# Optimization experiments

Hardware: AMD Instinct MI355X
Metric: run time of the kernel (lower is better)

Reference implementation:

```python
import jax, jax.numpy as jnp
import numpy as np

N = 100000
E = 1600000
IN_DIM = 128
HID_DIM = 128
NUM_CLASSES = 40


def setup_inputs() -> dict:
    key = jax.random.key(0)
    k1, k2, k3, k4, k5, k6 = jax.random.split(key, 6)
    x = jax.random.normal(k1, (N, IN_DIM), dtype=jnp.float32)
    e = jax.random.randint(k2, (2, E), 0, N, dtype=jnp.int64)
    s1 = 1.0 / np.sqrt(IN_DIM)
    s2 = 1.0 / np.sqrt(HID_DIM)
    W1 = jax.random.uniform(k3, (IN_DIM, HID_DIM), jnp.float32, -s1, s1)
    b1 = jax.random.uniform(k4, (HID_DIM,), jnp.float32, -s1, s1)
    W2 = jax.random.uniform(k5, (HID_DIM, NUM_CLASSES), jnp.float32, -s2, s2)
    b2 = jax.random.uniform(k6, (NUM_CLASSES,), jnp.float32, -s2, s2)
    return {"x": x, "e": e, "W1": W1, "b1": b1, "W2": W2, "b2": b2}


def _gcn_conv(x, src, dst, norm, W, b, n):
    # linear transform first (PyG GCNConv), then normalized aggregation
    h = x @ W                                    # [N, d_out]
    out = jax.ops.segment_sum(h[src] * norm[:, None], dst, num_segments=n)
    return out + b


def reference(x, e, W1, b1, W2, b2):
    n = x.shape[0]
    loop = jnp.arange(n, dtype=e.dtype)
    src = jnp.concatenate([e[0], loop])          # add self-loops
    dst = jnp.concatenate([e[1], loop])
    deg = jax.ops.segment_sum(jnp.ones_like(dst, dtype=x.dtype), dst, num_segments=n)
    d_inv_sqrt = deg ** -0.5                     # deg >= 1 due to self-loops
    norm = d_inv_sqrt[src] * d_inv_sqrt[dst]     # symmetric normalization
    h = jax.nn.relu(_gcn_conv(x, src, dst, norm, W1, b1, n))
    return _gcn_conv(h, src, dst, norm, W2, b2, n)
```

## Files before the change

kernel.cpp:

```cpp
#include <hip/hip_runtime.h>


typedef unsigned int u32;
typedef unsigned short u16;
typedef __attribute__((ext_vector_type(8))) short short8;
typedef __attribute__((ext_vector_type(4))) float floatx4;

#define CHUNK 8192

static __device__ inline u16 f2bf(float f) {
    u32 u = __float_as_uint(f);
    return (u16)((u + 0x7FFFu + ((u >> 16) & 1u)) >> 16);
}
static __device__ inline u32 pack2(float a, float b) {
    return (u32)f2bf(a) | ((u32)f2bf(b) << 16);
}
static __device__ inline float bflo(u32 u) { return __uint_as_float(u << 16); }
static __device__ inline float bfhi(u32 u) { return __uint_as_float(u & 0xffff0000u); }

__global__ void k_detect(const int* __restrict__ e32, int* __restrict__ flag) {
    int t = threadIdx.x;
    if (e32[2 * t + 1] != 0) atomicOr(flag, 1);
}

__global__ void k_prepW(const float* __restrict__ W1, const float* __restrict__ W2,
                        u16* __restrict__ WTb, u16* __restrict__ W2Tb) {
    int id = blockIdx.x * 256 + threadIdx.x;
    if (id < 16384) {
        int k = id >> 7, c = id & 127;
        WTb[c * 128 + k] = f2bf(W1[id]);
    } else {
        int id2 = id - 16384;
        if (id2 < 6144) {
            int c = id2 >> 7, k = id2 & 127;
            W2Tb[id2] = f2bf(c < 40 ? W2[k * 40 + c] : 0.f);
        }
    }
}

__global__ __launch_bounds__(256) void k_hist(const void* __restrict__ e_raw,
                                              const int* __restrict__ flag,
                                              int* __restrict__ histG,
                                              int E, int NB, int NC) {
    __shared__ int h[512];
    int c = blockIdx.x;
    int t = threadIdx.x;
    h[t] = 0; h[t + 256] = 0;
    __syncthreads();
    int j0 = c * CHUNK;
    int j1 = min(E, j0 + CHUNK);
    bool is64 = (*flag == 0);
    for (int j = j0 + t; j < j1; j += 256) {
        int d = is64 ? (int)((const long long*)e_raw)[E + j]
                     : ((const int*)e_raw)[E + j];
        atomicAdd(&h[d >> 8], 1);
    }
    __syncthreads();
    for (int b = t; b < NB; b += 256) histG[(size_t)b * NC + c] = h[b];
}

__global__ void k_scan1(const int* __restrict__ in, int* __restrict__ out,
                        int* __restrict__ bsum, int n) {
    __shared__ int sh[256];
    int i = blockIdx.x * 256 + threadIdx.x;
    int v = (i < n) ? in[i] : 0;
    sh[threadIdx.x] = v;
    __syncthreads();
    for (int off = 1; off < 256; off <<= 1) {
        int t = (threadIdx.x >= off) ? sh[threadIdx.x - off] : 0;
        __syncthreads();
        sh[threadIdx.x] += t;
        __syncthreads();
    }
    if (i < n) out[i] = sh[threadIdx.x] - v;
    if (threadIdx.x == 255) bsum[blockIdx.x] = sh[255];
}

__global__ void k_scan2(int* __restrict__ bsum, int nb) {
    __shared__ int sh[512];
    int t = threadIdx.x;
    int v = (t < nb) ? bsum[t] : 0;
    sh[t] = v;
    __syncthreads();
    for (int off = 1; off < 512; off <<= 1) {
        int u = (t >= off) ? sh[t - off] : 0;
        __syncthreads();
        sh[t] += u;
        __syncthreads();
    }
    if (t < nb) bsum[t] = sh[t] - v;
}

__global__ void k_scan3(int* __restrict__ out, const int* __restrict__ bsum, int n) {
    int i = blockIdx.x * 256 + threadIdx.x;
    if (i < n) out[i] += bsum[blockIdx.x];
}

__global__ __launch_bounds__(256) void k_place(const void* __restrict__ e_raw,
                                               const int* __restrict__ flag,
                                               const int* __restrict__ histOff,
                                               u32* __restrict__ tmp,
                                               int E, int NB, int NC) {
    __shared__ int cur[512];
    int c = blockIdx.x;
    int t = threadIdx.x;
    for (int b = t; b < NB; b += 256) cur[b] = histOff[(size_t)b * NC + c];
    __syncthreads();
    int j0 = c * CHUNK;
    int j1 = min(E, j0 + CHUNK);
    bool is64 = (*flag == 0);
    for (int j = j0 + t; j < j1; j += 256) {
        int s, d;
        if (is64) {
            s = (int)((const long long*)e_raw)[j];
            d = (int)((const long long*)e_raw)[E + j];
        } else {
            s = ((const int*)e_raw)[j];
            d = ((const int*)e_raw)[E + j];
        }
        int pos = atomicAdd(&cur[d >> 8], 1);
        tmp[pos] = (u32)s | ((u32)(d & 255) << 24);
    }
}

__global__ __launch_bounds__(256) void k_deg(const u32* __restrict__ tmp,
                                             const int* __restrict__ histOff,
                                             int* __restrict__ degI,
                                             float* __restrict__ dinv,
                                             int n, int NB, int NC, int E) {
    __shared__ int cnt[256];
    int b = blockIdx.x;
    int t = threadIdx.x;
    cnt[t] = 0;
    __syncthreads();
    int seg0 = histOff[(size_t)b * NC];
    int seg1 = (b + 1 < NB) ? histOff[(size_t)(b + 1) * NC] : E;
    for (int j = seg0 + t; j < seg1; j += 256) atomicAdd(&cnt[tmp[j] >> 24], 1);
    __syncthreads();
    int node = b * 256 + t;
    if (node < n) {
        degI[node] = cnt[t];
        dinv[node] = rsqrtf((float)cnt[t] + 1.0f);
    }
}

__global__ __launch_bounds__(256) void k_bsort(const u32* __restrict__ tmp,
                                               const int* __restrict__ rs,
                                               int* __restrict__ eSrc, int n, int E) {
    __shared__ int rsl[257];
    __shared__ int cur[256];
    int base = blockIdx.x * 256;
    int t = threadIdx.x;
    int node = base + t;
    rsl[t] = (node < n) ? rs[node] : E;
    cur[t] = 0;
    if (t == 0) rsl[256] = (base + 256 < n) ? rs[base + 256] : E;
    __syncthreads();
    int seg0 = rsl[0];
    int seg1 = rsl[256];
    for (int j = seg0 + t; j < seg1; j += 256) {
        u32 rec = tmp[j];
        int dl = rec >> 24;
        int s = (int)(rec & 0x00FFFFFFu);
        int pos = rsl[dl] + atomicAdd(&cur[dl], 1);
        eSrc[pos] = s;
    }
}

__global__ __launch_bounds__(256) void k_gemm1(const float* __restrict__ X,
                                               const u16* __restrict__ WTb,
                                               const float* __restrict__ dinv,
                                               u16* __restrict__ H1s, int n) {
    __shared__ u32 As[64 * 68];
    __shared__ u32 Bs[128 * 68];
    const int tid = threadIdx.x;
    const int row0 = blockIdx.x * 64;
#pragma unroll
    for (int it = 0; it < 8; it++) {
        int i = tid + it * 256;
        int r = i >> 5;
        int c4 = (i & 31) << 2;
        int gr = row0 + r;
        float4 v = make_float4(0.f, 0.f, 0.f, 0.f);
        if (gr < n) v = *(const float4*)(X + (size_t)gr * 128 + c4);
        uint2 p;
        p.x = pack2(v.x, v.y);
        p.y = pack2(v.z, v.w);
        *(uint2*)&As[r * 68 + (c4 >> 1)] = p;
    }
#pragma unroll
    for (int it = 0; it < 8; it++) {
        int i = tid + it * 256;
        int r = i >> 4;
        int c4 = (i & 15) << 2;
        *(uint4*)&Bs[r * 68 + c4] =
            *(const uint4*)((const u32*)WTb + (size_t)r * 64 + c4);
    }
    __syncthreads();

    const int lane = tid & 63;
    const int wave = tid >> 6;
    const int wr = wave >> 1;
    const int wc = wave & 1;
    const int mrow = lane & 15;
    const int quad = lane >> 4;

    floatx4 acc[2][4] = {};
    for (int k0 = 0; k0 < 128; k0 += 32) {
        int koff = (k0 >> 1) + quad * 4;
        short8 a[2], b[4];
#pragma unroll
        for (int i = 0; i < 2; i++)
            a[i] = *(const short8*)&As[((wr * 2 + i) * 16 + mrow) * 68 + koff];
#pragma unroll
        for (int j = 0; j < 4; j++)
            b[j] = *(const short8*)&Bs[((wc * 4 + j) * 16 + mrow) * 68 + koff];
#pragma unroll
        for (int i = 0; i < 2; i++)
#pragma unroll
            for (int j = 0; j < 4; j++)
                acc[i][j] = __builtin_amdgcn_mfma_f32_16x16x32_bf16(
                    a[i], b[j], acc[i][j], 0, 0, 0);
    }
#pragma unroll
    for (int i = 0; i < 2; i++) {
        int gr0 = row0 + (wr * 2 + i) * 16 + quad * 4;
        float dv[4];
#pragma unroll
        for (int rg = 0; rg < 4; rg++)
            dv[rg] = (gr0 + rg < n) ? dinv[gr0 + rg] : 0.f;
#pragma unroll
        for (int j = 0; j < 4; j++) {
            int gcol = (wc * 4 + j) * 16 + mrow;
#pragma unroll
            for (int rg = 0; rg < 4; rg++) {
                int grow = gr0 + rg;
                if (grow < n)
                    H1s[(size_t)grow * 128 + gcol] = f2bf(dv[rg] * acc[i][j][rg]);
            }
        }
    }
}

__global__ __launch_bounds__(256) void k_gemm2(const u32* __restrict__ A1b,
                                               const u16* __restrict__ W2Tb,
                                               const float* __restrict__ dinv,
                                               u16* __restrict__ H2s, int n) {
    __shared__ u32 As[64 * 68];
    __shared__ u32 Bs[48 * 68];
    const int tid = threadIdx.x;
    const int row0 = blockIdx.x * 64;
#pragma unroll
    for (int it = 0; it < 4; it++) {
        int i = tid + it * 256;
        int r = i >> 4;
        int c4 = (i & 15) << 2;
        int gr = row0 + r;
        uint4 v = make_uint4(0u, 0u, 0u, 0u);
        if (gr < n) v = *(const uint4*)(A1b + (size_t)gr * 64 + c4);
        *(uint4*)&As[r * 68 + c4] = v;
    }
#pragma unroll
    for (int it = 0; it < 3; it++) {
        int i = tid + it * 256;
        int r = i >> 4;
        int c4 = (i & 15) << 2;
        *(uint4*)&Bs[r * 68 + c4] =
            *(const uint4*)((const u32*)W2Tb + (size_t)r * 64 + c4);
    }
    __syncthreads();

    const int lane = tid & 63;
    const int wave = tid >> 6;
    const int mrow = lane & 15;
    const int quad = lane >> 4;

    floatx4 acc[3] = {};
    for (int k0 = 0; k0 < 128; k0 += 32) {
        int koff = (k0 >> 1) + quad * 4;
        short8 a = *(const short8*)&As[(wave * 16 + mrow) * 68 + koff];
#pragma unroll
        for (int j = 0; j < 3; j++) {
            short8 b = *(const short8*)&Bs[(j * 16 + mrow) * 68 + koff];
            acc[j] = __builtin_amdgcn_mfma_f32_16x16x32_bf16(a, b, acc[j], 0, 0, 0);
        }
    }
    int gr0 = row0 + wave * 16 + quad * 4;
    float dv[4];
#pragma unroll
    for (int rg = 0; rg < 4; rg++)
        dv[rg] = (gr0 + rg < n) ? dinv[gr0 + rg] : 0.f;
#pragma unroll
    for (int j = 0; j < 3; j++) {
        int gcol = j * 16 + mrow;
        if (gcol < 40) {
#pragma unroll
            for (int rg = 0; rg < 4; rg++) {
                int grow = gr0 + rg;
                if (grow < n)
                    H2s[(size_t)grow * 40 + gcol] = f2bf(dv[rg] * acc[j][rg]);
            }
        }
    }
}

__global__ __launch_bounds__(256) void k_gather128(
    const u32* __restrict__ Hb, const int* __restrict__ rs,
    const int* __restrict__ degI, const int* __restrict__ eSrc,
    const float* __restrict__ dinv, const float* __restrict__ b1,
    u32* __restrict__ outb, int n) {
    int wave = threadIdx.x >> 6;
    int lane = threadIdx.x & 63;
    int node = blockIdx.x * 4 + wave;
    if (node >= n) return;
    int start = rs[node];
    int deg = degI[node];
    float ax = 0.f, ay = 0.f;
    for (int base = 0; base < deg; base += 64) {
        int mS = 0;
        if (base + lane < deg) mS = eSrc[start + base + lane];
        int cnt = min(64, deg - base);
        int t = 0;
        for (; t + 4 <= cnt; t += 4) {
            int s0 = __shfl(mS, t + 0), s1 = __shfl(mS, t + 1);
            int s2 = __shfl(mS, t + 2), s3 = __shfl(mS, t + 3);
            u32 u0 = Hb[(size_t)s0 * 64 + lane];
            u32 u1 = Hb[(size_t)s1 * 64 + lane];
            u32 u2 = Hb[(size_t)s2 * 64 + lane];
            u32 u3 = Hb[(size_t)s3 * 64 + lane];
            ax += bflo(u0); ay += bfhi(u0);
            ax += bflo(u1); ay += bfhi(u1);
            ax += bflo(u2); ay += bfhi(u2);
            ax += bflo(u3); ay += bfhi(u3);
        }
        for (; t < cnt; t++) {
            int s = __shfl(mS, t);
            u32 u = Hb[(size_t)s * 64 + lane];
            ax += bflo(u); ay += bfhi(u);
        }
    }
    float di = dinv[node];
    u32 us = Hb[(size_t)node * 64 + lane];
    float2 bv = *(const float2*)(b1 + lane * 2);
    float rx = fmaxf(fmaf(di, ax + bflo(us), bv.x), 0.f);
    float ry = fmaxf(fmaf(di, ay + bfhi(us), bv.y), 0.f);
    outb[(size_t)node * 64 + lane] = pack2(rx, ry);
}

__global__ __launch_bounds__(256) void k_gather40(
    const u32* __restrict__ H2b, const int* __restrict__ rs,
    const int* __restrict__ degI, const int* __restrict__ eSrc,
    const float* __restrict__ dinv, const float* __restrict__ b2,
    float* __restrict__ out, int n) {
    int wave = threadIdx.x >> 6;
    int lane = threadIdx.x & 63;
    int node = blockIdx.x * 4 + wave;
    if (node >= n) return;
    int start = rs[node];
    int deg = degI[node];
    int g = lane / 20;
    int l = lane - g * 20;
    float ax = 0.f, ay = 0.f;
    for (int base = 0; base < deg; base += 64) {
        int mS = 0;
        if (base + lane < deg) mS = eSrc[start + base + lane];
        int cnt = min(64, deg - base);
        for (int t = 0; t < cnt; t += 3) {
            int e = (t + g) & 63;
            int s = __shfl(mS, e);
            if (g < 3 && t + g < cnt) {
                u32 u = H2b[(size_t)s * 20 + l];
                ax += bflo(u);
                ay += bfhi(u);
            }
        }
    }
    float x1 = __shfl(ax, (lane + 20) & 63), y1 = __shfl(ay, (lane + 20) & 63);
    float x2 = __shfl(ax, (lane + 40) & 63), y2 = __shfl(ay, (lane + 40) & 63);
    if (lane < 20) {
        float di = dinv[node];
        u32 u = H2b[(size_t)node * 20 + l];
        float2 bv = *(const float2*)(b2 + l * 2);
        float ox = fmaf(di, ax + x1 + x2 + bflo(u), bv.x);
        float oy = fmaf(di, ay + y1 + y2 + bfhi(u), bv.y);
        *(float2*)(out + (size_t)node * 40 + l * 2) = make_float2(ox, oy);
    }
}

extern "C" void kernel_launch(void* const* d_in, const int* in_sizes, int n_in,
                              void* d_out, int out_size, void* d_ws, size_t ws_size,
                              hipStream_t stream) {
    const float* x  = (const float*)d_in[0];
    const void*  e  = d_in[1];
    const float* W1 = (const float*)d_in[2];
    const float* b1 = (const float*)d_in[3];
    const float* W2 = (const float*)d_in[4];
    const float* b2 = (const float*)d_in[5];
    float* out = (float*)d_out;

    const int n = in_sizes[0] / 128;
    const int E = in_sizes[1] / 2;
    const int NB = (n + 255) / 256;
    const int NC = (E + CHUNK - 1) / CHUNK;
    const int NH = NB * NC;
    const int nbH = (NH + 255) / 256;
    const int nbN = (n + 255) / 256;

    int*   flag    = (int*)d_ws;
    int*   degI    = flag + 1;
    int*   rs      = degI + n;
    int*   bsumH   = rs + n;
    int*   bsumN   = bsumH + 512;
    float* dinv    = (float*)(bsumN + 512);
    int*   histG   = (int*)(dinv + n);
    int*   histOff = histG + NH;
    size_t off = (size_t)((char*)(histOff + NH) - (char*)d_ws);
    off = (off + 15) & ~(size_t)15;
    u16*   WTb    = (u16*)((char*)d_ws + off);
    u16*   W2Tb   = WTb + 16384;
    off = (size_t)((char*)(W2Tb + 6144) - (char*)d_ws);
    off = (off + 15) & ~(size_t)15;
    u32*   tmp    = (u32*)((char*)d_ws + off);
    int*   eSrc   = (int*)(tmp + (size_t)E);
    u16*   H1s    = (u16*)(eSrc + (size_t)E);
    u32*   H1b    = (u32*)H1s;
    u32*   A1b    = (u32*)(H1s + (size_t)n * 128);
    u16*   H2s    = (u16*)(A1b + (size_t)n * 64);
    u32*   H2b    = (u32*)H2s;

    hipMemsetAsync(flag, 0, 4, stream);
    k_prepW<<<88, 256, 0, stream>>>(W1, W2, WTb, W2Tb);
    k_detect<<<1, 256, 0, stream>>>((const int*)e, flag);

    k_hist<<<NC, 256, 0, stream>>>(e, flag, histG, E, NB, NC);
    k_scan1<<<nbH, 256, 0, stream>>>(histG, histOff, bsumH, NH);
    k_scan2<<<1, 512, 0, stream>>>(bsumH, nbH);
    k_scan3<<<nbH, 256, 0, stream>>>(histOff, bsumH, NH);
    k_place<<<NC, 256, 0, stream>>>(e, flag, histOff, tmp, E, NB, NC);

    k_deg<<<NB, 256, 0, stream>>>(tmp, histOff, degI, dinv, n, NB, NC, E);
    k_scan1<<<nbN, 256, 0, stream>>>(degI, rs, bsumN, n);
    k_scan2<<<1, 512, 0, stream>>>(bsumN, nbN);
    k_scan3<<<nbN, 256, 0, stream>>>(rs, bsumN, n);
    k_bsort<<<NB, 256, 0, stream>>>(tmp, rs, eSrc, n, E);

    k_gemm1<<<(n + 63) / 64, 256, 0, stream>>>(x, WTb, dinv, H1s, n);
    k_gather128<<<(n + 3) / 4, 256, 0, stream>>>(H1b, rs, degI, eSrc, dinv,
                                                 b1, A1b, n);
    k_gemm2<<<(n + 63) / 64, 256, 0, stream>>>(A1b, W2Tb, dinv, H2s, n);
    k_gather40<<<(n + 3) / 4, 256, 0, stream>>>(H2b, rs, degI, eSrc, dinv,
                                                b2, out, n);
}
```

Measured before the change: 337.8 us.

## Fuse histogram with GEMM1, inline dtype detection, fold scans into degree kernel

```diff
diff --git a/kernel.cpp b/kernel.cpp
--- a/kernel.cpp
+++ b/kernel.cpp
@@ -6,7 +6,7 @@
 typedef __attribute__((ext_vector_type(8))) short short8;
 typedef __attribute__((ext_vector_type(4))) float floatx4;
 
-#define CHUNK 8192
+#define CHUNK 4096
 
 static __device__ inline u16 f2bf(float f) {
     u32 u = __float_as_uint(f);
@@ -18,9 +18,9 @@
 static __device__ inline float bflo(u32 u) { return __uint_as_float(u << 16); }
 static __device__ inline float bfhi(u32 u) { return __uint_as_float(u & 0xffff0000u); }
 
-__global__ void k_detect(const int* __restrict__ e32, int* __restrict__ flag) {
-    int t = threadIdx.x;
-    if (e32[2 * t + 1] != 0) atomicOr(flag, 1);
+static __device__ inline bool detect_is64(const int* e32, int lane) {
+    bool nz = e32[2 * lane + 1] != 0;
+    return __ballot(nz) == 0ull;
 }
 
 __global__ void k_prepW(const float* __restrict__ W1, const float* __restrict__ W2,
@@ -38,25 +38,94 @@
     }
 }
 
-__global__ __launch_bounds__(256) void k_hist(const void* __restrict__ e_raw,
-                                              const int* __restrict__ flag,
-                                              int* __restrict__ histG,
-                                              int E, int NB, int NC) {
-    __shared__ int h[512];
-    int c = blockIdx.x;
-    int t = threadIdx.x;
-    h[t] = 0; h[t + 256] = 0;
-    __syncthreads();
-    int j0 = c * CHUNK;
-    int j1 = min(E, j0 + CHUNK);
-    bool is64 = (*flag == 0);
-    for (int j = j0 + t; j < j1; j += 256) {
-        int d = is64 ? (int)((const long long*)e_raw)[E + j]
-                     : ((const int*)e_raw)[E + j];
-        atomicAdd(&h[d >> 8], 1);
-    }
-    __syncthreads();
-    for (int b = t; b < NB; b += 256) histG[(size_t)b * NC + c] = h[b];
+__global__ __launch_bounds__(256) void k_front(const void* __restrict__ e_raw,
+                                               int E, int NC, int NB,
+                                               int* __restrict__ histG,
+                                               const float* __restrict__ X,
+                                               const u16* __restrict__ WTb,
+                                               u16* __restrict__ H1s, int n) {
+    __shared__ u32 smem[64 * 68 + 128 * 68];
+    const int tid = threadIdx.x;
+    if ((int)blockIdx.x < NC) {
+        int* h = (int*)smem;
+        h[tid] = 0; h[tid + 256] = 0;
+        __syncthreads();
+        const int* e32 = (const int*)e_raw;
+        bool is64 = detect_is64(e32, tid & 63);
+        int c = blockIdx.x;
+        int j0 = c * CHUNK, j1 = min(E, j0 + CHUNK);
+        for (int j = j0 + tid; j < j1; j += 256) {
+            int d = is64 ? (int)((const long long*)e_raw)[E + j] : e32[E + j];
+            atomicAdd(&h[d >> 8], 1);
+        }
+        __syncthreads();
+        for (int b = tid; b < NB; b += 256) histG[(size_t)b * NC + c] = h[b];
+        return;
+    }
+    u32* As = smem;
+    u32* Bs = smem + 64 * 68;
+    const int row0 = ((int)blockIdx.x - NC) * 64;
+#pragma unroll
+    for (int it = 0; it < 8; it++) {
+        int i = tid + it * 256;
+        int r = i >> 5;
+        int c4 = (i & 31) << 2;
+        int gr = row0 + r;
+        float4 v = make_float4(0.f, 0.f, 0.f, 0.f);
+        if (gr < n) v = *(const float4*)(X + (size_t)gr * 128 + c4);
+        uint2 p;
+        p.x = pack2(v.x, v.y);
+        p.y = pack2(v.z, v.w);
+        *(uint2*)&As[r * 68 + (c4 >> 1)] = p;
+    }
+#pragma unroll
+    for (int it = 0; it < 8; it++) {
+        int i = tid + it * 256;
+        int r = i >> 4;
+        int c4 = (i & 15) << 2;
+        *(uint4*)&Bs[r * 68 + c4] =
+            *(const uint4*)((const u32*)WTb + (size_t)r * 64 + c4);
+    }
+    __syncthreads();
+
+    const int lane = tid & 63;
+    const int wave = tid >> 6;
+    const int wr = wave >> 1;
+    const int wc = wave & 1;
+    const int mrow = lane & 15;
+    const int quad = lane >> 4;
+
+    floatx4 acc[2][4] = {};
+    for (int k0 = 0; k0 < 128; k0 += 32) {
+        int koff = (k0 >> 1) + quad * 4;
+        short8 a[2], b[4];
+#pragma unroll
+        for (int i = 0; i < 2; i++)
+            a[i] = *(const short8*)&As[((wr * 2 + i) * 16 + mrow) * 68 + koff];
+#pragma unroll
+        for (int j = 0; j < 4; j++)
+            b[j] = *(const short8*)&Bs[((wc * 4 + j) * 16 + mrow) * 68 + koff];
+#pragma unroll
+        for (int i = 0; i < 2; i++)
+#pragma unroll
+            for (int j = 0; j < 4; j++)
+                acc[i][j] = __builtin_amdgcn_mfma_f32_16x16x32_bf16(
+                    a[i], b[j], acc[i][j], 0, 0, 0);
+    }
+#pragma unroll
+    for (int i = 0; i < 2; i++) {
+        int gr0 = row0 + (wr * 2 + i) * 16 + quad * 4;
+#pragma unroll
+        for (int j = 0; j < 4; j++) {
+            int gcol = (wc * 4 + j) * 16 + mrow;
+#pragma unroll
+            for (int rg = 0; rg < 4; rg++) {
+                int grow = gr0 + rg;
+                if (grow < n)
+                    H1s[(size_t)grow * 128 + gcol] = f2bf(acc[i][j][rg]);
+            }
+        }
+    }
 }
 
 __global__ void k_scan1(const int* __restrict__ in, int* __restrict__ out,
@@ -77,12 +146,12 @@
 }
 
 __global__ void k_scan2(int* __restrict__ bsum, int nb) {
-    __shared__ int sh[512];
+    __shared__ int sh[1024];
     int t = threadIdx.x;
     int v = (t < nb) ? bsum[t] : 0;
     sh[t] = v;
     __syncthreads();
-    for (int off = 1; off < 512; off <<= 1) {
+    for (int off = 1; off < 1024; off <<= 1) {
         int u = (t >= off) ? sh[t - off] : 0;
         __syncthreads();
         sh[t] += u;
@@ -91,32 +160,30 @@
     if (t < nb) bsum[t] = sh[t] - v;
 }
 
-__global__ void k_scan3(int* __restrict__ out, const int* __restrict__ bsum, int n) {
-    int i = blockIdx.x * 256 + threadIdx.x;
-    if (i < n) out[i] += bsum[blockIdx.x];
-}
-
 __global__ __launch_bounds__(256) void k_place(const void* __restrict__ e_raw,
-                                               const int* __restrict__ flag,
                                                const int* __restrict__ histOff,
+                                               const int* __restrict__ bsumH,
                                                u32* __restrict__ tmp,
                                                int E, int NB, int NC) {
     __shared__ int cur[512];
     int c = blockIdx.x;
     int t = threadIdx.x;
-    for (int b = t; b < NB; b += 256) cur[b] = histOff[(size_t)b * NC + c];
-    __syncthreads();
-    int j0 = c * CHUNK;
-    int j1 = min(E, j0 + CHUNK);
-    bool is64 = (*flag == 0);
+    for (int b = t; b < NB; b += 256) {
+        int idx = b * NC + c;
+        cur[b] = histOff[idx] + bsumH[idx >> 8];
+    }
+    __syncthreads();
+    const int* e32 = (const int*)e_raw;
+    bool is64 = detect_is64(e32, t & 63);
+    int j0 = c * CHUNK, j1 = min(E, j0 + CHUNK);
     for (int j = j0 + t; j < j1; j += 256) {
         int s, d;
         if (is64) {
             s = (int)((const long long*)e_raw)[j];
             d = (int)((const long long*)e_raw)[E + j];
         } else {
-            s = ((const int*)e_raw)[j];
-            d = ((const int*)e_raw)[E + j];
+            s = e32[j];
+            d = e32[E + j];
         }
         int pos = atomicAdd(&cur[d >> 8], 1);
         tmp[pos] = (u32)s | ((u32)(d & 255) << 24);
@@ -125,22 +192,40 @@
 
 __global__ __launch_bounds__(256) void k_deg(const u32* __restrict__ tmp,
                                              const int* __restrict__ histOff,
+                                             const int* __restrict__ bsumH,
                                              int* __restrict__ degI,
                                              float* __restrict__ dinv,
+                                             int* __restrict__ rs,
                                              int n, int NB, int NC, int E) {
     __shared__ int cnt[256];
+    __shared__ int sh[256];
     int b = blockIdx.x;
     int t = threadIdx.x;
     cnt[t] = 0;
     __syncthreads();
-    int seg0 = histOff[(size_t)b * NC];
-    int seg1 = (b + 1 < NB) ? histOff[(size_t)(b + 1) * NC] : E;
+    int i0 = b * NC;
+    int seg0 = histOff[i0] + bsumH[i0 >> 8];
+    int seg1 = E;
+    if (b + 1 < NB) {
+        int i1 = (b + 1) * NC;
+        seg1 = histOff[i1] + bsumH[i1 >> 8];
+    }
     for (int j = seg0 + t; j < seg1; j += 256) atomicAdd(&cnt[tmp[j] >> 24], 1);
     __syncthreads();
+    int v = cnt[t];
+    sh[t] = v;
+    __syncthreads();
+    for (int off = 1; off < 256; off <<= 1) {
+        int u = (t >= off) ? sh[t - off] : 0;
+        __syncthreads();
+        sh[t] += u;
+        __syncthreads();
+    }
     int node = b * 256 + t;
     if (node < n) {
-        degI[node] = cnt[t];
-        dinv[node] = rsqrtf((float)cnt[t] + 1.0f);
+        degI[node] = v;
+        dinv[node] = rsqrtf((float)v + 1.0f);
+        rs[node] = seg0 + sh[t] - v;
     }
 }
 
@@ -164,143 +249,6 @@
         int s = (int)(rec & 0x00FFFFFFu);
         int pos = rsl[dl] + atomicAdd(&cur[dl], 1);
         eSrc[pos] = s;
-    }
-}
-
-__global__ __launch_bounds__(256) void k_gemm1(const float* __restrict__ X,
-                                               const u16* __restrict__ WTb,
-                                               const float* __restrict__ dinv,
-                                               u16* __restrict__ H1s, int n) {
-    __shared__ u32 As[64 * 68];
-    __shared__ u32 Bs[128 * 68];
-    const int tid = threadIdx.x;
-    const int row0 = blockIdx.x * 64;
-#pragma unroll
-    for (int it = 0; it < 8; it++) {
-        int i = tid + it * 256;
-        int r = i >> 5;
-        int c4 = (i & 31) << 2;
-        int gr = row0 + r;
-        float4 v = make_float4(0.f, 0.f, 0.f, 0.f);
-        if (gr < n) v = *(const float4*)(X + (size_t)gr * 128 + c4);
-        uint2 p;
-        p.x = pack2(v.x, v.y);
-        p.y = pack2(v.z, v.w);
-        *(uint2*)&As[r * 68 + (c4 >> 1)] = p;
-    }
-#pragma unroll
-    for (int it = 0; it < 8; it++) {
-        int i = tid + it * 256;
-        int r = i >> 4;
-        int c4 = (i & 15) << 2;
-        *(uint4*)&Bs[r * 68 + c4] =
-            *(const uint4*)((const u32*)WTb + (size_t)r * 64 + c4);
-    }
-    __syncthreads();
-
-    const int lane = tid & 63;
-    const int wave = tid >> 6;
-    const int wr = wave >> 1;
-    const int wc = wave & 1;
-    const int mrow = lane & 15;
-    const int quad = lane >> 4;
-
-    floatx4 acc[2][4] = {};
-    for (int k0 = 0; k0 < 128; k0 += 32) {
-        int koff = (k0 >> 1) + quad * 4;
-        short8 a[2], b[4];
-#pragma unroll
-        for (int i = 0; i < 2; i++)
-            a[i] = *(const short8*)&As[((wr * 2 + i) * 16 + mrow) * 68 + koff];
-#pragma unroll
-        for (int j = 0; j < 4; j++)
-            b[j] = *(const short8*)&Bs[((wc * 4 + j) * 16 + mrow) * 68 + koff];
-#pragma unroll
-        for (int i = 0; i < 2; i++)
-#pragma unroll
-            for (int j = 0; j < 4; j++)
-                acc[i][j] = __builtin_amdgcn_mfma_f32_16x16x32_bf16(
-                    a[i], b[j], acc[i][j], 0, 0, 0);
-    }
-#pragma unroll
-    for (int i = 0; i < 2; i++) {
-        int gr0 = row0 + (wr * 2 + i) * 16 + quad * 4;
-        float dv[4];
-#pragma unroll
-        for (int rg = 0; rg < 4; rg++)
-            dv[rg] = (gr0 + rg < n) ? dinv[gr0 + rg] : 0.f;
-#pragma unroll
-        for (int j = 0; j < 4; j++) {
-            int gcol = (wc * 4 + j) * 16 + mrow;
-#pragma unroll
-            for (int rg = 0; rg < 4; rg++) {
-                int grow = gr0 + rg;
-                if (grow < n)
-                    H1s[(size_t)grow * 128 + gcol] = f2bf(dv[rg] * acc[i][j][rg]);
-            }
-        }
-    }
-}
-
-__global__ __launch_bounds__(256) void k_gemm2(const u32* __restrict__ A1b,
-                                               const u16* __restrict__ W2Tb,
-                                               const float* __restrict__ dinv,
-                                               u16* __restrict__ H2s, int n) {
-    __shared__ u32 As[64 * 68];
-    __shared__ u32 Bs[48 * 68];
-    const int tid = threadIdx.x;
-    const int row0 = blockIdx.x * 64;
-#pragma unroll
-    for (int it = 0; it < 4; it++) {
-        int i = tid + it * 256;
-        int r = i >> 4;
-        int c4 = (i & 15) << 2;
-        int gr = row0 + r;
-        uint4 v = make_uint4(0u, 0u, 0u, 0u);
-        if (gr < n) v = *(const uint4*)(A1b + (size_t)gr * 64 + c4);
-        *(uint4*)&As[r * 68 + c4] = v;
-    }
-#pragma unroll
-    for (int it = 0; it < 3; it++) {
-        int i = tid + it * 256;
-        int r = i >> 4;
-        int c4 = (i & 15) << 2;
-        *(uint4*)&Bs[r * 68 + c4] =
-            *(const uint4*)((const u32*)W2Tb + (size_t)r * 64 + c4);
-    }
-    __syncthreads();
-
-    const int lane = tid & 63;
-    const int wave = tid >> 6;
-    const int mrow = lane & 15;
-    const int quad = lane >> 4;
-
-    floatx4 acc[3] = {};
-    for (int k0 = 0; k0 < 128; k0 += 32) {
-        int koff = (k0 >> 1) + quad * 4;
-        short8 a = *(const short8*)&As[(wave * 16 + mrow) * 68 + koff];
-#pragma unroll
-        for (int j = 0; j < 3; j++) {
-            short8 b = *(const short8*)&Bs[(j * 16 + mrow) * 68 + koff];
-            acc[j] = __builtin_amdgcn_mfma_f32_16x16x32_bf16(a, b, acc[j], 0, 0, 0);
-        }
-    }
-    int gr0 = row0 + wave * 16 + quad * 4;
-    float dv[4];
-#pragma unroll
-    for (int rg = 0; rg < 4; rg++)
-        dv[rg] = (gr0 + rg < n) ? dinv[gr0 + rg] : 0.f;
-#pragma unroll
-    for (int j = 0; j < 3; j++) {
-        int gcol = j * 16 + mrow;
-        if (gcol < 40) {
-#pragma unroll
-            for (int rg = 0; rg < 4; rg++) {
-                int grow = gr0 + rg;
-                if (grow < n)
-                    H2s[(size_t)grow * 40 + gcol] = f2bf(dv[rg] * acc[j][rg]);
-            }
-        }
     }
 }
 
@@ -318,33 +266,113 @@
     float ax = 0.f, ay = 0.f;
     for (int base = 0; base < deg; base += 64) {
         int mS = 0;
-        if (base + lane < deg) mS = eSrc[start + base + lane];
+        float mW = 0.f;
+        if (base + lane < deg) { mS = eSrc[start + base + lane]; mW = dinv[mS]; }
         int cnt = min(64, deg - base);
         int t = 0;
-        for (; t + 4 <= cnt; t += 4) {
+        for (; t + 8 <= cnt; t += 8) {
             int s0 = __shfl(mS, t + 0), s1 = __shfl(mS, t + 1);
             int s2 = __shfl(mS, t + 2), s3 = __shfl(mS, t + 3);
+            int s4 = __shfl(mS, t + 4), s5 = __shfl(mS, t + 5);
+            int s6 = __shfl(mS, t + 6), s7 = __shfl(mS, t + 7);
+            float w0 = __shfl(mW, t + 0), w1 = __shfl(mW, t + 1);
+            float w2 = __shfl(mW, t + 2), w3 = __shfl(mW, t + 3);
+            float w4 = __shfl(mW, t + 4), w5 = __shfl(mW, t + 5);
+            float w6 = __shfl(mW, t + 6), w7 = __shfl(mW, t + 7);
             u32 u0 = Hb[(size_t)s0 * 64 + lane];
             u32 u1 = Hb[(size_t)s1 * 64 + lane];
             u32 u2 = Hb[(size_t)s2 * 64 + lane];
             u32 u3 = Hb[(size_t)s3 * 64 + lane];
-            ax += bflo(u0); ay += bfhi(u0);
-            ax += bflo(u1); ay += bfhi(u1);
-            ax += bflo(u2); ay += bfhi(u2);
-            ax += bflo(u3); ay += bfhi(u3);
+            u32 u4 = Hb[(size_t)s4 * 64 + lane];
+            u32 u5 = Hb[(size_t)s5 * 64 + lane];
+            u32 u6 = Hb[(size_t)s6 * 64 + lane];
+            u32 u7 = Hb[(size_t)s7 * 64 + lane];
+            ax = fmaf(w0, bflo(u0), ax); ay = fmaf(w0, bfhi(u0), ay);
+            ax = fmaf(w1, bflo(u1), ax); ay = fmaf(w1, bfhi(u1), ay);
+            ax = fmaf(w2, bflo(u2), ax); ay = fmaf(w2, bfhi(u2), ay);
+            ax = fmaf(w3, bflo(u3), ax); ay = fmaf(w3, bfhi(u3), ay);
+            ax = fmaf(w4, bflo(u4), ax); ay = fmaf(w4, bfhi(u4), ay);
+            ax = fmaf(w5, bflo(u5), ax); ay = fmaf(w5, bfhi(u5), ay);
+            ax = fmaf(w6, bflo(u6), ax); ay = fmaf(w6, bfhi(u6), ay);
+            ax = fmaf(w7, bflo(u7), ax); ay = fmaf(w7, bfhi(u7), ay);
         }
         for (; t < cnt; t++) {
             int s = __shfl(mS, t);
+            float w = __shfl(mW, t);
             u32 u = Hb[(size_t)s * 64 + lane];
-            ax += bflo(u); ay += bfhi(u);
+            ax = fmaf(w, bflo(u), ax); ay = fmaf(w, bfhi(u), ay);
         }
     }
     float di = dinv[node];
     u32 us = Hb[(size_t)node * 64 + lane];
+    float inx = fmaf(di, bflo(us), ax);
+    float iny = fmaf(di, bfhi(us), ay);
     float2 bv = *(const float2*)(b1 + lane * 2);
-    float rx = fmaxf(fmaf(di, ax + bflo(us), bv.x), 0.f);
-    float ry = fmaxf(fmaf(di, ay + bfhi(us), bv.y), 0.f);
+    float rx = fmaxf(fmaf(di, inx, bv.x), 0.f);
+    float ry = fmaxf(fmaf(di, iny, bv.y), 0.f);
     outb[(size_t)node * 64 + lane] = pack2(rx, ry);
+}
+
+__global__ __launch_bounds__(256) void k_gemm2(const u32* __restrict__ A1b,
+                                               const u16* __restrict__ W2Tb,
+                                               const float* __restrict__ dinv,
+                                               u16* __restrict__ H2s, int n) {
+    __shared__ u32 As[64 * 68];
+    __shared__ u32 Bs[48 * 68];
+    const int tid = threadIdx.x;
+    const int row0 = blockIdx.x * 64;
+#pragma unroll
+    for (int it = 0; it < 4; it++) {
+        int i = tid + it * 256;
+        int r = i >> 4;
+        int c4 = (i & 15) << 2;
+        int gr = row0 + r;
+        uint4 v = make_uint4(0u, 0u, 0u, 0u);
+        if (gr < n) v = *(const uint4*)(A1b + (size_t)gr * 64 + c4);
+        *(uint4*)&As[r * 68 + c4] = v;
+    }
+#pragma unroll
+    for (int it = 0; it < 3; it++) {
+        int i = tid + it * 256;
+        int r = i >> 4;
+        int c4 = (i & 15) << 2;
+        *(uint4*)&Bs[r * 68 + c4] =
+            *(const uint4*)((const u32*)W2Tb + (size_t)r * 64 + c4);
+    }
+    __syncthreads();
+
+    const int lane = tid & 63;
+    const int wave = tid >> 6;
+    const int mrow = lane & 15;
+    const int quad = lane >> 4;
+
+    floatx4 acc[3] = {};
+    for (int k0 = 0; k0 < 128; k0 += 32) {
+        int koff = (k0 >> 1) + quad * 4;
+        short8 a = *(const short8*)&As[(wave * 16 + mrow) * 68 + koff];
+#pragma unroll
+        for (int j = 0; j < 3; j++) {
+            short8 b = *(const short8*)&Bs[(j * 16 + mrow) * 68 + koff];
+            acc[j] = __builtin_amdgcn_mfma_f32_16x16x32_bf16(a, b, acc[j], 0, 0, 0);
+        }
+    }
+    int gr0 = row0 + wave * 16 + quad * 4;
+    float dv[4];
+#pragma unroll
+    for (int rg = 0; rg < 4; rg++)
+        dv[rg] = (gr0 + rg < n) ? dinv[gr0 + rg] : 0.f;
+#pragma unroll
+    for (int j = 0; j < 3; j++) {
+        int gcol = j * 16 + mrow;
+        if (gcol < 40) {
+#pragma unroll
+            for (int rg = 0; rg < 4; rg++) {
+                int grow = gr0 + rg;
+                if (grow < n)
+                    H2s[(size_t)grow * 40 + gcol] = f2bf(dv[rg] * acc[j][rg]);
+            }
+        }
+    }
 }
 
 __global__ __launch_bounds__(256) void k_gather40(
@@ -404,14 +432,12 @@
     const int NC = (E + CHUNK - 1) / CHUNK;
     const int NH = NB * NC;
     const int nbH = (NH + 255) / 256;
-    const int nbN = (n + 255) / 256;
-
-    int*   flag    = (int*)d_ws;
-    int*   degI    = flag + 1;
+    const int G1 = (n + 63) / 64;
+
+    int*   degI    = (int*)d_ws;
     int*   rs      = degI + n;
     int*   bsumH   = rs + n;
-    int*   bsumN   = bsumH + 512;
-    float* dinv    = (float*)(bsumN + 512);
+    float* dinv    = (float*)(bsumH + 1024);
     int*   histG   = (int*)(dinv + n);
     int*   histOff = histG + NH;
     size_t off = (size_t)((char*)(histOff + NH) - (char*)d_ws);
@@ -428,23 +454,17 @@
     u16*   H2s    = (u16*)(A1b + (size_t)n * 64);
     u32*   H2b    = (u32*)H2s;
 
-    hipMemsetAsync(flag, 0, 4, stream);
     k_prepW<<<88, 256, 0, stream>>>(W1, W2, WTb, W2Tb);
-    k_detect<<<1, 256, 0, stream>>>((const int*)e, flag);
-
-    k_hist<<<NC, 256, 0, stream>>>(e, flag, histG, E, NB, NC);
+    k_front<<<NC + G1, 256, 0, stream>>>(e, E, NC, NB, histG, x, WTb, H1s, n);
+
     k_scan1<<<nbH, 256, 0, stream>>>(histG, histOff, bsumH, NH);
-    k_scan2<<<1, 512, 0, stream>>>(bsumH, nbH);
-    k_scan3<<<nbH, 256, 0, stream>>>(histOff, bsumH, NH);
-    k_place<<<NC, 256, 0, stream>>>(e, flag, histOff, tmp, E, NB, NC);
-
-    k_deg<<<NB, 256, 0, stream>>>(tmp, histOff, degI, dinv, n, NB, NC, E);
-    k_scan1<<<nbN, 256, 0, stream>>>(degI, rs, bsumN, n);
-    k_scan2<<<1, 512, 0, stream>>>(bsumN, nbN);
-    k_scan3<<<nbN, 256, 0, stream>>>(rs, bsumN, n);
+    k_scan2<<<1, 1024, 0, stream>>>(bsumH, nbH);
+    k_place<<<NC, 256, 0, stream>>>(e, histOff, bsumH, tmp, E, NB, NC);
+
+    k_deg<<<NB, 256, 0, stream>>>(tmp, histOff, bsumH, degI, dinv, rs,
+                                  n, NB, NC, E);
     k_bsort<<<NB, 256, 0, stream>>>(tmp, rs, eSrc, n, E);
 
-    k_gemm1<<<(n + 63) / 64, 256, 0, stream>>>(x, WTb, dinv, H1s, n);
     k_gather128<<<(n + 3) / 4, 256, 0, stream>>>(H1b, rs, degI, eSrc, dinv,
                                                  b1, A1b, n);
     k_gemm2<<<(n + 63) / 64, 256, 0, stream>>>(A1b, W2Tb, dinv, H2s, n);
```

New measurement: 318.7 us. -5.7%, faster.
